# Kernel tuning notes

Measured on AMD Instinct MI355X. Metric: run time of the kernel, lower is better.

The kernel has to match this reference:

```python
import jax, jax.numpy as jnp
import numpy as np

B, T, DIN, D = 8, 2048, 512, 1024
LN_EPS = 1e-5


def setup_inputs() -> dict:
    key = jax.random.key(0)
    ks = jax.random.split(key, 4)
    x = jax.random.normal(ks[0], (B, T, DIN), dtype=jnp.float32)
    Wd = jax.random.normal(ks[1], (DIN, D), dtype=jnp.float32) * (1.0 / np.sqrt(DIN))
    bd = jnp.zeros((D,), jnp.float32)  # nn.init.constant_(delta_proj.bias, 0)
    Wb = jax.random.normal(ks[2], (DIN, D), dtype=jnp.float32) * (1.0 / np.sqrt(DIN))
    bb = jax.random.normal(ks[3], (D,), dtype=jnp.float32) * 0.02
    A_log = jnp.log(jnp.linspace(1.0, 16.0, D, dtype=jnp.float32))
    threshold = jnp.ones((D,), jnp.float32)
    gamma = jnp.ones((D,), jnp.float32)
    beta = jnp.zeros((D,), jnp.float32)
    return {"x": x, "Wd": Wd, "bd": bd, "Wb": Wb, "bb": bb,
            "A_log": A_log, "threshold": threshold, "gamma": gamma, "beta": beta}


def reference(x, Wd, bd, Wb, bb, A_log, threshold, gamma, beta):
    # Input-dependent discretization (parallel over B,T)
    delta = jax.nn.softplus(jnp.einsum('btc,cd->btd', x, Wd) + bd)   # [B,T,D]
    b_step = delta * (jnp.einsum('btc,cd->btd', x, Wb) + bb)          # [B,T,D]
    A = jnp.exp(A_log)                                                # [D]
    a_step = jnp.exp(-delta * A)                                      # [B,T,D]

    # Sequential spiking scan with multiplicative threshold reset (fp32)
    def step(h, ab):
        a, b = ab
        h = a * h + b
        s = (h - threshold > 0).astype(h.dtype)  # spike (no grad path)
        h = h * (1.0 - s)                        # reset
        return h, (h, s)

    aT = jnp.swapaxes(a_step, 0, 1)  # [T,B,D]
    bT = jnp.swapaxes(b_step, 0, 1)
    h0 = jnp.zeros((x.shape[0], A.shape[0]), a_step.dtype)
    _, (hT, sT) = jax.lax.scan(step, h0, (aT, bT))
    h_post = jnp.swapaxes(hT, 0, 1)  # [B,T,D]
    spikes = jnp.swapaxes(sT, 0, 1)

    # LayerNorm over last dim (biased variance, as torch)
    mu = jnp.mean(h_post, axis=-1, keepdims=True)
    var = jnp.mean(jnp.square(h_post - mu), axis=-1, keepdims=True)
    out = (h_post - mu) * jax.lax.rsqrt(var + LN_EPS) * gamma + beta
    return out, spikes
```

## Files before the change

### kernel.cpp

```cpp
#include <hip/hip_runtime.h>
#include <math.h>

#define BB   8
#define TT   2048
#define CIN  512
#define DD   1024
#define MM   (BB * TT)

constexpr int BM = 128;
constexpr int BN = 64;
constexpr int BK = 16;

#define NCHUNK 16
#define CLEN   (TT / NCHUNK)
#define WARM   128
#define PF     16

__device__ __forceinline__ float softplus_f(float z) {
    return fmaxf(z, 0.f) + log1pf(expf(-fabsf(z)));
}

__global__ __launch_bounds__(256) void k1_gemm_act(
    const float* __restrict__ x,
    const float* __restrict__ Wd,
    const float* __restrict__ Wb,
    const float* __restrict__ bd,
    const float* __restrict__ bb,
    const float* __restrict__ A_log,
    float* __restrict__ a_out,
    float* __restrict__ b_out)
{
    __shared__ float xs[BK][BM + 4];
    __shared__ float wds[BK][BN];
    __shared__ float wbs[BK][BN];

    const int tid = threadIdx.x;
    const int n0  = blockIdx.x * BN;
    const int m0  = blockIdx.y * BM;
    const int tx  = tid & 15;
    const int ty  = tid >> 4;

    const int lm = tid >> 1;
    const int lk = (tid & 1) * 8;
    const int wr = tid >> 4;
    const int wc = (tid & 15) * 4;

    float accd[8][4], accb[8][4];
#pragma unroll
    for (int r = 0; r < 8; ++r)
#pragma unroll
        for (int c = 0; c < 4; ++c) { accd[r][c] = 0.f; accb[r][c] = 0.f; }

    const float* xp  = x + (size_t)(m0 + lm) * CIN + lk;
    const float* wdp = Wd + (size_t)wr * DD + n0 + wc;
    const float* wbp = Wb + (size_t)wr * DD + n0 + wc;
    float4 xva = *(const float4*)(xp);
    float4 xvb = *(const float4*)(xp + 4);
    float4 wd0 = *(const float4*)(wdp);
    float4 wb0 = *(const float4*)(wbp);

    for (int k0 = 0; k0 < CIN; k0 += BK) {
        __syncthreads();
        xs[lk + 0][lm] = xva.x;  xs[lk + 1][lm] = xva.y;
        xs[lk + 2][lm] = xva.z;  xs[lk + 3][lm] = xva.w;
        xs[lk + 4][lm] = xvb.x;  xs[lk + 5][lm] = xvb.y;
        xs[lk + 6][lm] = xvb.z;  xs[lk + 7][lm] = xvb.w;
        *(float4*)&wds[wr][wc] = wd0;
        *(float4*)&wbs[wr][wc] = wb0;
        __syncthreads();

        const int kn = k0 + BK;
        if (kn < CIN) {
            xva = *(const float4*)(xp + kn);
            xvb = *(const float4*)(xp + kn + 4);
            wd0 = *(const float4*)(wdp + (size_t)kn * DD);
            wb0 = *(const float4*)(wbp + (size_t)kn * DD);
        }

#pragma unroll
        for (int kk = 0; kk < BK; ++kk) {
            float4 xa  = *(const float4*)&xs[kk][ty * 8];
            float4 xa2 = *(const float4*)&xs[kk][ty * 8 + 4];
            float4 d0  = *(const float4*)&wds[kk][tx * 4];
            float4 c0  = *(const float4*)&wbs[kk][tx * 4];
            float xr[8] = {xa.x, xa.y, xa.z, xa.w, xa2.x, xa2.y, xa2.z, xa2.w};
            float wd[4] = {d0.x, d0.y, d0.z, d0.w};
            float wb[4] = {c0.x, c0.y, c0.z, c0.w};
#pragma unroll
            for (int r = 0; r < 8; ++r) {
                const float xi = xr[r];
#pragma unroll
                for (int c = 0; c < 4; ++c) {
                    accd[r][c] = fmaf(xi, wd[c], accd[r][c]);
                    accb[r][c] = fmaf(xi, wb[c], accb[r][c]);
                }
            }
        }
    }

    const int nc0 = n0 + tx * 4;
    float4 bdq = *(const float4*)(bd + nc0);
    float4 bbq = *(const float4*)(bb + nc0);
    float4 alq = *(const float4*)(A_log + nc0);
    const float* bdv = (const float*)&bdq;
    const float* bbv = (const float*)&bbq;
    float Aq[4] = {expf(alq.x), expf(alq.y), expf(alq.z), expf(alq.w)};

#pragma unroll
    for (int r = 0; r < 8; ++r) {
        const int m = m0 + ty * 8 + r;
        float av[4], bv[4];
#pragma unroll
        for (int j = 0; j < 4; ++j) {
            float zd    = accd[r][j] + bdv[j];
            float delta = softplus_f(zd);
            float zb    = accb[r][j] + bbv[j];
            av[j] = expf(-delta * Aq[j]);
            bv[j] = delta * zb;
        }
        *(float4*)(a_out + (size_t)m * DD + nc0) = make_float4(av[0], av[1], av[2], av[3]);
        *(float4*)(b_out + (size_t)m * DD + nc0) = make_float4(bv[0], bv[1], bv[2], bv[3]);
    }
}

__global__ __launch_bounds__(64) void k2_scan(
    const float* __restrict__ a,
    const float* __restrict__ b,
    const float* __restrict__ thr,
    float* __restrict__ hout,
    float* __restrict__ sout)
{
    const int gid   = blockIdx.x * 64 + threadIdx.x;
    const int batch = gid >> 10;
    const int d     = gid & (DD - 1);
    const float th  = thr[d];
    const size_t base = (size_t)batch * TT * DD + d;

    const int chunk = blockIdx.y;
    const int t0    = chunk * CLEN;
    const int nwarm = (chunk == 0) ? 0 : WARM;
    const int tw    = t0 - nwarm;
    const int nwb   = nwarm / PF;
    const int ntot  = nwb + CLEN / PF;

    const float* ap = a + base + (size_t)tw * DD;
    const float* bp = b + base + (size_t)tw * DD;
    float* hp = hout + base + (size_t)t0 * DD;
    float* sp = sout + base + (size_t)t0 * DD;

    float a0[PF], b0[PF], a1[PF], b1[PF];
#pragma unroll
    for (int j = 0; j < PF; ++j) { a0[j] = ap[(size_t)j * DD]; b0[j] = bp[(size_t)j * DD]; }
    ap += (size_t)PF * DD; bp += (size_t)PF * DD;

    float h = 0.f;
    for (int i = 0; i < ntot; i += 2) {
#pragma unroll
        for (int j = 0; j < PF; ++j) { a1[j] = ap[(size_t)j * DD]; b1[j] = bp[(size_t)j * DD]; }
        ap += (size_t)PF * DD; bp += (size_t)PF * DD;

        if (i >= nwb) {
#pragma unroll
            for (int j = 0; j < PF; ++j) {
                h = fmaf(a0[j], h, b0[j]);
                const bool spike = (h - th) > 0.f;
                *sp = spike ? 1.f : 0.f;
                h = spike ? 0.f : h;
                *hp = h;
                hp += DD; sp += DD;
            }
        } else {
#pragma unroll
            for (int j = 0; j < PF; ++j) {
                h = fmaf(a0[j], h, b0[j]);
                h = ((h - th) > 0.f) ? 0.f : h;
            }
        }

        if (i + 2 < ntot) {
#pragma unroll
            for (int j = 0; j < PF; ++j) { a0[j] = ap[(size_t)j * DD]; b0[j] = bp[(size_t)j * DD]; }
            ap += (size_t)PF * DD; bp += (size_t)PF * DD;
        }

        if (i + 1 >= nwb) {
#pragma unroll
            for (int j = 0; j < PF; ++j) {
                h = fmaf(a1[j], h, b1[j]);
                const bool spike = (h - th) > 0.f;
                *sp = spike ? 1.f : 0.f;
                h = spike ? 0.f : h;
                *hp = h;
                hp += DD; sp += DD;
            }
        } else {
#pragma unroll
            for (int j = 0; j < PF; ++j) {
                h = fmaf(a1[j], h, b1[j]);
                h = ((h - th) > 0.f) ? 0.f : h;
            }
        }
    }
}

__global__ __launch_bounds__(256) void k3_ln(
    float* __restrict__ h,
    const float* __restrict__ gamma,
    const float* __restrict__ beta)
{
    const int row = blockIdx.x;
    const int tid = threadIdx.x;
    const int lane = tid & 63;
    const int wid  = tid >> 6;

    __shared__ float red[4];
    __shared__ float bc[2];

    float* rp = h + (size_t)row * DD + tid * 4;
    float4 v = *(const float4*)rp;

    float s = v.x + v.y + v.z + v.w;
#pragma unroll
    for (int off = 32; off > 0; off >>= 1) s += __shfl_down(s, off);
    if (lane == 0) red[wid] = s;
    __syncthreads();
    if (tid == 0) bc[0] = (red[0] + red[1] + red[2] + red[3]) * (1.0f / DD);
    __syncthreads();
    const float mu = bc[0];

    float dx = v.x - mu, dy = v.y - mu, dz = v.z - mu, dw = v.w - mu;
    float ss = dx * dx + dy * dy + dz * dz + dw * dw;
#pragma unroll
    for (int off = 32; off > 0; off >>= 1) ss += __shfl_down(ss, off);
    __syncthreads();
    if (lane == 0) red[wid] = ss;
    __syncthreads();
    if (tid == 0) bc[1] = (red[0] + red[1] + red[2] + red[3]) * (1.0f / DD);
    __syncthreads();
    const float inv = 1.0f / sqrtf(bc[1] + 1e-5f);

    float4 g  = *(const float4*)(gamma + tid * 4);
    float4 be = *(const float4*)(beta + tid * 4);
    float4 o;
    o.x = dx * inv * g.x + be.x;
    o.y = dy * inv * g.y + be.y;
    o.z = dz * inv * g.z + be.z;
    o.w = dw * inv * g.w + be.w;
    *(float4*)rp = o;
}

extern "C" void kernel_launch(void* const* d_in, const int* in_sizes, int n_in,
                              void* d_out, int out_size, void* d_ws, size_t ws_size,
                              hipStream_t stream) {
    const float* x     = (const float*)d_in[0];
    const float* Wd    = (const float*)d_in[1];
    const float* bd    = (const float*)d_in[2];
    const float* Wb    = (const float*)d_in[3];
    const float* bb    = (const float*)d_in[4];
    const float* A_log = (const float*)d_in[5];
    const float* thr   = (const float*)d_in[6];
    const float* gamma = (const float*)d_in[7];
    const float* beta  = (const float*)d_in[8];

    float* out    = (float*)d_out;
    float* spikes = out + (size_t)MM * DD;
    float* a_ws   = (float*)d_ws;
    float* b_ws   = a_ws + (size_t)MM * DD;

    dim3 g1(DD / BN, MM / BM);
    k1_gemm_act<<<g1, 256, 0, stream>>>(x, Wd, Wb, bd, bb, A_log, a_ws, b_ws);

    dim3 g2(BB * DD / 64, NCHUNK);
    k2_scan<<<g2, 64, 0, stream>>>(a_ws, b_ws, thr, out, spikes);

    k3_ln<<<MM, 256, 0, stream>>>(out, gamma, beta);
}
```

Baseline: 684.2 us.

## Replace shared-memory tiled GEMM with register-only row-broadcast kernel

The projection GEMM drops its LDS-tiled 128x64 outer-product scheme. In its place, each thread owns one output column and accumulates 16 rows, reading x directly from global memory as wavefront-uniform broadcast loads and W as coalesced column loads. This removes the shared-memory staging and barriers. The cost is much lower arithmetic intensity: W is re-read for every 16-row block and x is re-read by 8 column blocks, so the GEMM leans more on cache bandwidth.

After: 873.6 us. 1.28x slower.

```diff
diff --git a/kernel.cpp b/kernel.cpp
--- a/kernel.cpp
+++ b/kernel.cpp
@@ -7,9 +7,7 @@
 #define DD   1024
 #define MM   (BB * TT)
 
-constexpr int BM = 128;
-constexpr int BN = 64;
-constexpr int BK = 16;
+#define K1_ROWS 16
 
 #define NCHUNK 16
 #define CLEN   (TT / NCHUNK)
@@ -20,7 +18,7 @@
     return fmaxf(z, 0.f) + log1pf(expf(-fabsf(z)));
 }
 
-__global__ __launch_bounds__(256) void k1_gemm_act(
+__global__ __launch_bounds__(128) void k1_gemm_act(
     const float* __restrict__ x,
     const float* __restrict__ Wd,
     const float* __restrict__ Wb,
@@ -30,96 +28,55 @@
     float* __restrict__ a_out,
     float* __restrict__ b_out)
 {
-    __shared__ float xs[BK][BM + 4];
-    __shared__ float wds[BK][BN];
-    __shared__ float wbs[BK][BN];
-
-    const int tid = threadIdx.x;
-    const int n0  = blockIdx.x * BN;
-    const int m0  = blockIdx.y * BM;
-    const int tx  = tid & 15;
-    const int ty  = tid >> 4;
-
-    const int lm = tid >> 1;
-    const int lk = (tid & 1) * 8;
-    const int wr = tid >> 4;
-    const int wc = (tid & 15) * 4;
-
-    float accd[8][4], accb[8][4];
-#pragma unroll
-    for (int r = 0; r < 8; ++r)
-#pragma unroll
-        for (int c = 0; c < 4; ++c) { accd[r][c] = 0.f; accb[r][c] = 0.f; }
-
-    const float* xp  = x + (size_t)(m0 + lm) * CIN + lk;
-    const float* wdp = Wd + (size_t)wr * DD + n0 + wc;
-    const float* wbp = Wb + (size_t)wr * DD + n0 + wc;
-    float4 xva = *(const float4*)(xp);
-    float4 xvb = *(const float4*)(xp + 4);
-    float4 wd0 = *(const float4*)(wdp);
-    float4 wb0 = *(const float4*)(wbp);
-
-    for (int k0 = 0; k0 < CIN; k0 += BK) {
-        __syncthreads();
-        xs[lk + 0][lm] = xva.x;  xs[lk + 1][lm] = xva.y;
-        xs[lk + 2][lm] = xva.z;  xs[lk + 3][lm] = xva.w;
-        xs[lk + 4][lm] = xvb.x;  xs[lk + 5][lm] = xvb.y;
-        xs[lk + 6][lm] = xvb.z;  xs[lk + 7][lm] = xvb.w;
-        *(float4*)&wds[wr][wc] = wd0;
-        *(float4*)&wbs[wr][wc] = wb0;
-        __syncthreads();
-
-        const int kn = k0 + BK;
-        if (kn < CIN) {
-            xva = *(const float4*)(xp + kn);
-            xvb = *(const float4*)(xp + kn + 4);
-            wd0 = *(const float4*)(wdp + (size_t)kn * DD);
-            wb0 = *(const float4*)(wbp + (size_t)kn * DD);
-        }
-
-#pragma unroll
-        for (int kk = 0; kk < BK; ++kk) {
-            float4 xa  = *(const float4*)&xs[kk][ty * 8];
-            float4 xa2 = *(const float4*)&xs[kk][ty * 8 + 4];
-            float4 d0  = *(const float4*)&wds[kk][tx * 4];
-            float4 c0  = *(const float4*)&wbs[kk][tx * 4];
-            float xr[8] = {xa.x, xa.y, xa.z, xa.w, xa2.x, xa2.y, xa2.z, xa2.w};
-            float wd[4] = {d0.x, d0.y, d0.z, d0.w};
-            float wb[4] = {c0.x, c0.y, c0.z, c0.w};
-#pragma unroll
-            for (int r = 0; r < 8; ++r) {
-                const float xi = xr[r];
-#pragma unroll
-                for (int c = 0; c < 4; ++c) {
-                    accd[r][c] = fmaf(xi, wd[c], accd[r][c]);
-                    accb[r][c] = fmaf(xi, wb[c], accb[r][c]);
-                }
+    const int c  = blockIdx.x & 7;
+    const int rb = blockIdx.x >> 3;
+    const int n  = c * 128 + threadIdx.x;
+    const int m0 = rb * K1_ROWS;
+
+    const float* xb  = x + (size_t)m0 * CIN;
+    const float* wdp = Wd + n;
+    const float* wbp = Wb + n;
+
+    float accd[K1_ROWS], accb[K1_ROWS];
+#pragma unroll
+    for (int r = 0; r < K1_ROWS; ++r) { accd[r] = 0.f; accb[r] = 0.f; }
+
+    for (int k0 = 0; k0 < CIN; k0 += 4) {
+        float4 xr[K1_ROWS];
+#pragma unroll
+        for (int r = 0; r < K1_ROWS; ++r)
+            xr[r] = *(const float4*)(xb + (size_t)r * CIN + k0);
+
+        float wdv[4], wbv[4];
+#pragma unroll
+        for (int kk = 0; kk < 4; ++kk) {
+            wdv[kk] = wdp[(size_t)(k0 + kk) * DD];
+            wbv[kk] = wbp[(size_t)(k0 + kk) * DD];
+        }
+
+#pragma unroll
+        for (int kk = 0; kk < 4; ++kk) {
+#pragma unroll
+            for (int r = 0; r < K1_ROWS; ++r) {
+                const float xi = ((const float*)&xr[r])[kk];
+                accd[r] = fmaf(xi, wdv[kk], accd[r]);
+                accb[r] = fmaf(xi, wbv[kk], accb[r]);
             }
         }
     }
 
-    const int nc0 = n0 + tx * 4;
-    float4 bdq = *(const float4*)(bd + nc0);
-    float4 bbq = *(const float4*)(bb + nc0);
-    float4 alq = *(const float4*)(A_log + nc0);
-    const float* bdv = (const float*)&bdq;
-    const float* bbv = (const float*)&bbq;
-    float Aq[4] = {expf(alq.x), expf(alq.y), expf(alq.z), expf(alq.w)};
-
-#pragma unroll
-    for (int r = 0; r < 8; ++r) {
-        const int m = m0 + ty * 8 + r;
-        float av[4], bv[4];
-#pragma unroll
-        for (int j = 0; j < 4; ++j) {
-            float zd    = accd[r][j] + bdv[j];
-            float delta = softplus_f(zd);
-            float zb    = accb[r][j] + bbv[j];
-            av[j] = expf(-delta * Aq[j]);
-            bv[j] = delta * zb;
-        }
-        *(float4*)(a_out + (size_t)m * DD + nc0) = make_float4(av[0], av[1], av[2], av[3]);
-        *(float4*)(b_out + (size_t)m * DD + nc0) = make_float4(bv[0], bv[1], bv[2], bv[3]);
+    const float bdv = bd[n];
+    const float bbv = bb[n];
+    const float Av  = expf(A_log[n]);
+
+#pragma unroll
+    for (int r = 0; r < K1_ROWS; ++r) {
+        const int m = m0 + r;
+        const float zd    = accd[r] + bdv;
+        const float delta = softplus_f(zd);
+        const float zb    = accb[r] + bbv;
+        a_out[(size_t)m * DD + n] = expf(-delta * Av);
+        b_out[(size_t)m * DD + n] = delta * zb;
     }
 }
 
@@ -267,8 +224,7 @@
     float* a_ws   = (float*)d_ws;
     float* b_ws   = a_ws + (size_t)MM * DD;
 
-    dim3 g1(DD / BN, MM / BM);
-    k1_gemm_act<<<g1, 256, 0, stream>>>(x, Wd, Wb, bd, bb, A_log, a_ws, b_ws);
+    k1_gemm_act<<<8 * (MM / K1_ROWS), 128, 0, stream>>>(x, Wd, Wb, bd, bb, A_log, a_ws, b_ws);
 
     dim3 g2(BB * DD / 64, NCHUNK);
     k2_scan<<<g2, 64, 0, stream>>>(a_ws, b_ws, thr, out, spikes);
```
